# Optimization experiments

Measured on AMD Instinct MI355X. Metric: run time of the kernel, lower is better.

Reference implementation:

```python
import jax, jax.numpy as jnp
import numpy as np

B, T, N, IN_DIM, H = 8, 16, 1024, 2, 128
HEADS, HD = 8, 16            # HEADS*HD == H (DGL GATConv head-concat)
SNP, SEQ_OUT, DEG = 4, 12, 8
NT = SNP * N                 # nodes per HSTG graph
CKPNT = [4, 7, 10, 13, 16]   # _generate_checkpoints(4, 16)
LRELU = 0.2


def _build_edges():
    # HSTG: per-snapshot spatial edges (random deg-8 adjacency + self-loops)
    # plus identity temporal edges t -> t+1 (uni-direction, non-dense, sync).
    rng = np.random.default_rng(0)
    src, dst = [], []
    ar = np.arange(N)
    for t in range(SNP):
        off = t * N
        src.append(rng.integers(0, N, size=N * DEG) + off)
        dst.append(np.repeat(ar, DEG) + off)
        src.append(ar + off)   # self-loops (keep every dst non-empty)
        dst.append(ar + off)
    for t in range(SNP - 1):
        src.append(ar + t * N)
        dst.append(ar + (t + 1) * N)
    return (jnp.asarray(np.concatenate(src), dtype=jnp.int32),
            jnp.asarray(np.concatenate(dst), dtype=jnp.int32))


def setup_inputs() -> dict:
    key = jax.random.key(0)
    ks = jax.random.split(key, 16)
    edge_src, edge_dst = _build_edges()
    rn = lambda k, s, sc: jax.random.normal(k, s, dtype=jnp.float32) * sc
    return {
        'inputs': rn(ks[0], (B, T, N, IN_DIM), 1.0),
        'W_in': rn(ks[1], (IN_DIM, H), 0.5),
        'b_in': jnp.zeros((H,), jnp.float32),
        'spatial_emb': rn(ks[2], (N, H), 0.05),
        'temporal_emb': rn(ks[3], (N, T), 0.05),
        'gat_w0': rn(ks[4], (H, HEADS * HD), 0.1),
        'gat_al0': rn(ks[5], (HEADS, HD), 0.1),
        'gat_ar0': rn(ks[6], (HEADS, HD), 0.1),
        'gat_b0': jnp.zeros((HEADS * HD,), jnp.float32),
        'gat_w1': rn(ks[7], (H, HEADS * HD), 0.1),
        'gat_al1': rn(ks[8], (HEADS, HD), 0.1),
        'gat_ar1': rn(ks[9], (HEADS, HD), 0.1),
        'gat_b1': jnp.zeros((HEADS * HD,), jnp.float32),
        'agg_q': rn(ks[10], (N, H), 0.1),
        'w_out1': rn(ks[11], (1, SEQ_OUT), 0.5),
        'b_out1': jnp.zeros((SEQ_OUT,), jnp.float32),
        'w_out2': rn(ks[12], (H, 1), 0.1),
        'b_out2': jnp.zeros((1,), jnp.float32),
        'edge_src': edge_src,
        'edge_dst': edge_dst,
    }


def _gat_layer(x, W, a_l, a_r, b, src, dst, activate):
    # x: [NT, H] node features of one graph
    feat = (x @ W).reshape(NT, HEADS, HD)
    el = jnp.sum(feat * a_l, axis=-1)                 # [NT, HEADS]
    er = jnp.sum(feat * a_r, axis=-1)
    e = jax.nn.leaky_relu(el[src] + er[dst], LRELU)    # [E, HEADS]
    m = jax.ops.segment_max(e, dst, num_segments=NT)
    w = jnp.exp(e - m[dst])
    s = jax.ops.segment_sum(w, dst, num_segments=NT)
    alpha = w / s[dst]
    out = jax.ops.segment_sum(feat[src] * alpha[..., None], dst, num_segments=NT)
    out = out.reshape(NT, HEADS * HD) + b
    return jax.nn.elu(out) if activate else out


def reference(inputs, W_in, b_in, spatial_emb, temporal_emb,
              gat_w0, gat_al0, gat_ar0, gat_b0,
              gat_w1, gat_al1, gat_ar1, gat_b1,
              agg_q, w_out1, b_out1, w_out2, b_out2,
              edge_src, edge_dst):
    # input projection + spatial/temporal embeddings
    x = inputs @ W_in + b_in                           # [B,T,N,H]
    x = x + spatial_emb                                # broadcast [N,H]
    x = x + temporal_emb.T[None, :, :, None]           # add temb[n,t] at [b,t,n,h]

    def gat(xb):  # xb: [NT,H], one sample of the batched block-diagonal graph
        h = _gat_layer(xb, gat_w0, gat_al0, gat_ar0, gat_b0, edge_src, edge_dst, True)
        return _gat_layer(h, gat_w1, gat_al1, gat_ar1, gat_b1, edge_src, edge_dst, False)
    gat_b = jax.vmap(gat)

    last = None
    left = 0
    for idx, right in enumerate(CKPNT):
        fs = x[:, left:right]                          # [B, snp or snp-1, N, H]
        if idx != 0:
            fs = jnp.concatenate([last, fs], axis=1)   # [B, SNP, N, H]
        residual = fs
        h = gat_b(fs.reshape(B, NT, H)).reshape(B, SNP, N, H)
        h = h + residual
        # Aggregator: per-node attention over the SNP snapshots -> [B,1,N,H]
        scores = jnp.einsum('btnh,nh->btn', h, agg_q)
        alpha = jax.nn.softmax(scores, axis=1)
        last = jnp.einsum('btn,btnh->bnh', alpha, h)[:, None]
        # LayerNorm over normalized_shape [1,N,H], no affine
        mu = jnp.mean(last, axis=(1, 2, 3), keepdims=True)
        var = jnp.var(last, axis=(1, 2, 3), keepdims=True)
        last = (last - mu) * jax.lax.rsqrt(var + 1e-5)
        left = right

    # decoder (meta_decode = False)
    t = jnp.transpose(last, (0, 3, 2, 1))              # [B,H,N,1]
    o = jax.nn.relu(t @ w_out1 + b_out1)               # [B,H,N,SEQ_OUT]
    o = jnp.transpose(o, (0, 3, 2, 1))                 # [B,SEQ_OUT,N,H]
    return o @ w_out2 + b_out2                         # [B,SEQ_OUT,N,1]
```

## Files before the change

kernel.cpp:

```cpp
#include <hip/hip_runtime.h>
#include <hip/hip_bf16.h>
#include <math.h>

constexpr int kB = 8;
constexpr int kT = 16;
constexpr int kN = 1024;
constexpr int kH = 128;
constexpr int kSNP = 4;
constexpr int kNT = kSNP * kN;
constexpr int kRows = kB * kNT;
constexpr int kSeqOut = 12;
constexpr float kLRelu = 0.2f;
constexpr int kEdgePerSnap = kN * 8 + kN;
constexpr int kSelfOff = kN * 8;
constexpr int kTempBase = kSNP * kEdgePerSnap;
constexpr int kStatsPerIter = kB * 16 * 16;

typedef __bf16 bf16x8 __attribute__((ext_vector_type(8)));
typedef float f32x4 __attribute__((ext_vector_type(4)));

__global__ void prep_w(const float* __restrict__ gw0, const float* __restrict__ gw1,
                       unsigned short* __restrict__ wbuf) {
  int tid = blockIdx.x * 256 + threadIdx.x;
  int layer = tid >> 14;
  int e = tid & 16383;
  int k = e >> 7, col = e & 127;
  const float* W = layer ? gw1 : gw0;
  float w = W[k * kH + col];
  unsigned int bits = __float_as_uint(w);
  unsigned short hi = (unsigned short)(bits >> 16);
  float hif = __uint_as_float(bits & 0xffff0000u);
  unsigned short lo = (unsigned short)(__float_as_uint(w - hif) >> 16);
  int s = k >> 5, q = (k >> 3) & 3, j = k & 7;
  int off = ((s * 4 + q) * kH + col) * 8 + j;
  wbuf[layer * 32768 + off] = hi;
  wbuf[layer * 32768 + 16384 + off] = lo;
}

__global__ void build_fs(const float* __restrict__ inputs, const float* __restrict__ W_in,
                         const float* __restrict__ b_in, const float* __restrict__ spatial,
                         const float* __restrict__ temporal, const float* __restrict__ last,
                         const float* __restrict__ stats, float* __restrict__ A,
                         int left, int first) {
  int blk = blockIdx.x;
  int b = blk & 7;
  int inner = blk >> 3;
  int idx4 = (b << 17) | (inner << 8) | threadIdx.x;
  int h4 = idx4 & 31;
  int n  = (idx4 >> 5) & 1023;
  int t  = (idx4 >> 15) & 3;
  float4 out;
  if (!first && t == 0) {
    float s1 = 0.f, s2 = 0.f;
    #pragma unroll
    for (int s = 0; s < 16; ++s) {
      s1 += stats[b * 256 + s * 16];
      s2 += stats[b * 256 + s * 16 + 1];
    }
    const float inv = 1.0f / (float)(kN * kH);
    float mu = s1 * inv;
    float var = s2 * inv - mu * mu;
    float sc = rsqrtf(var + 1e-5f);
    float4 v = *(const float4*)(last + ((size_t)(b * kN + n)) * kH + h4 * 4);
    out.x = (v.x - mu) * sc; out.y = (v.y - mu) * sc;
    out.z = (v.z - mu) * sc; out.w = (v.w - mu) * sc;
  } else {
    int tg = left + t - (first ? 0 : 1);
    float2 iv = *(const float2*)(inputs + ((size_t)((b * kT + tg) * kN + n)) * 2);
    float tv = temporal[n * kT + tg];
    float4 w0 = *(const float4*)(W_in + h4 * 4);
    float4 w1 = *(const float4*)(W_in + kH + h4 * 4);
    float4 bb = *(const float4*)(b_in + h4 * 4);
    float4 sp = *(const float4*)(spatial + n * kH + h4 * 4);
    out.x = iv.x * w0.x + iv.y * w1.x + bb.x + sp.x + tv;
    out.y = iv.x * w0.y + iv.y * w1.y + bb.y + sp.y + tv;
    out.z = iv.x * w0.z + iv.y * w1.z + bb.z + sp.z + tv;
    out.w = iv.x * w0.w + iv.y * w1.w + bb.w + sp.w + tv;
  }
  *(float4*)(A + (size_t)idx4 * 4) = out;
}

__launch_bounds__(256)
__global__ void gemm_mfma(const float* __restrict__ In, const unsigned short* __restrict__ Wh,
                          const unsigned short* __restrict__ Wl,
                          const float* __restrict__ gal, const float* __restrict__ gar,
                          float* __restrict__ Out, float* __restrict__ elp,
                          float* __restrict__ erp) {
  __shared__ unsigned short AhL[64 * 128];
  __shared__ unsigned short AlL[64 * 128];
  int tid = threadIdx.x;
  int lane = tid & 63, wid = tid >> 6;
  int blk = blockIdx.x;
  int rowblk = ((blk & 7) << 6) | (blk >> 3);
  int blockRow0 = rowblk * 64;
  int colL = lane & 15;
  int q = lane >> 4;

  bf16x8 bh[2][4], bl[2][4];
  #pragma unroll
  for (int c = 0; c < 2; ++c) {
    int col = wid * 32 + c * 16 + colL;
    #pragma unroll
    for (int s = 0; s < 4; ++s) {
      int off = ((s * 4 + q) * kH + col) * 8;
      bh[c][s] = *(const bf16x8*)(Wh + off);
      bl[c][s] = *(const bf16x8*)(Wl + off);
    }
  }

  const float* Ablk = In + (size_t)blockRow0 * kH;
  #pragma unroll
  for (int itn = 0; itn < 8; ++itn) {
    int fid = itn * 256 + tid;
    int row = fid >> 5, kq = fid & 31;
    float4 v = *(const float4*)(Ablk + (size_t)row * kH + kq * 4);
    ushort4 hi, lo;
    unsigned int bx = __float_as_uint(v.x);
    hi.x = bx >> 16; lo.x = __float_as_uint(v.x - __uint_as_float(bx & 0xffff0000u)) >> 16;
    unsigned int by = __float_as_uint(v.y);
    hi.y = by >> 16; lo.y = __float_as_uint(v.y - __uint_as_float(by & 0xffff0000u)) >> 16;
    unsigned int bz = __float_as_uint(v.z);
    hi.z = bz >> 16; lo.z = __float_as_uint(v.z - __uint_as_float(bz & 0xffff0000u)) >> 16;
    unsigned int bw = __float_as_uint(v.w);
    hi.w = bw >> 16; lo.w = __float_as_uint(v.w - __uint_as_float(bw & 0xffff0000u)) >> 16;
    int boff = (row * 256 + kq * 8) ^ ((row & 7) << 4);
    *(ushort4*)((char*)AhL + boff) = hi;
    *(ushort4*)((char*)AlL + boff) = lo;
  }
  __syncthreads();

  f32x4 acc[4][2];
  #pragma unroll
  for (int rb = 0; rb < 4; ++rb)
    #pragma unroll
    for (int c = 0; c < 2; ++c) acc[rb][c] = (f32x4){0.f, 0.f, 0.f, 0.f};

  #pragma unroll
  for (int s = 0; s < 4; ++s) {
    bf16x8 ah[4], alr[4];
    #pragma unroll
    for (int rb = 0; rb < 4; ++rb) {
      int row = rb * 16 + colL;
      int boff = (row * 256 + s * 64 + q * 16) ^ ((row & 7) << 4);
      ah[rb]  = *(const bf16x8*)((const char*)AhL + boff);
      alr[rb] = *(const bf16x8*)((const char*)AlL + boff);
    }
    #pragma unroll
    for (int c = 0; c < 2; ++c) {
      #pragma unroll
      for (int rb = 0; rb < 4; ++rb)
        acc[rb][c] = __builtin_amdgcn_mfma_f32_16x16x32_bf16(ah[rb], bh[c][s], acc[rb][c], 0, 0, 0);
      #pragma unroll
      for (int rb = 0; rb < 4; ++rb)
        acc[rb][c] = __builtin_amdgcn_mfma_f32_16x16x32_bf16(alr[rb], bh[c][s], acc[rb][c], 0, 0, 0);
      #pragma unroll
      for (int rb = 0; rb < 4; ++rb)
        acc[rb][c] = __builtin_amdgcn_mfma_f32_16x16x32_bf16(ah[rb], bl[c][s], acc[rb][c], 0, 0, 0);
    }
  }

  int rquad = q * 4;
  #pragma unroll
  for (int c = 0; c < 2; ++c) {
    int h = wid * 2 + c;
    float alv = gal[h * 16 + colL];
    float arv = gar[h * 16 + colL];
    int col = wid * 32 + c * 16 + colL;
    #pragma unroll
    for (int rb = 0; rb < 4; ++rb) {
      f32x4 a = acc[rb][c];
      int row0g = blockRow0 + rb * 16 + rquad;
      #pragma unroll
      for (int r = 0; r < 4; ++r)
        Out[(size_t)(row0g + r) * kH + col] = a[r];
      float e0 = a[0] * alv, e1 = a[1] * alv, e2 = a[2] * alv, e3 = a[3] * alv;
      float f0 = a[0] * arv, f1 = a[1] * arv, f2 = a[2] * arv, f3 = a[3] * arv;
      #pragma unroll
      for (int m = 1; m < 16; m <<= 1) {
        e0 += __shfl_xor(e0, m, 64); e1 += __shfl_xor(e1, m, 64);
        e2 += __shfl_xor(e2, m, 64); e3 += __shfl_xor(e3, m, 64);
        f0 += __shfl_xor(f0, m, 64); f1 += __shfl_xor(f1, m, 64);
        f2 += __shfl_xor(f2, m, 64); f3 += __shfl_xor(f3, m, 64);
      }
      if (colL == 0) {
        elp[(size_t)(row0g + 0) * 8 + h] = e0;
        elp[(size_t)(row0g + 1) * 8 + h] = e1;
        elp[(size_t)(row0g + 2) * 8 + h] = e2;
        elp[(size_t)(row0g + 3) * 8 + h] = e3;
        erp[(size_t)(row0g + 0) * 8 + h] = f0;
        erp[(size_t)(row0g + 1) * 8 + h] = f1;
        erp[(size_t)(row0g + 2) * 8 + h] = f2;
        erp[(size_t)(row0g + 3) * 8 + h] = f3;
      }
    }
  }
}

__launch_bounds__(256)
__global__ void agg0_kernel(const float* __restrict__ feat, const float* __restrict__ el,
                            const float* __restrict__ er, const int* __restrict__ esrc,
                            const float* __restrict__ bias, float* __restrict__ outp) {
  int blk = blockIdx.x;
  int b = blk & 7;
  int grp = blk >> 3;
  int tid = threadIdx.x;
  int wave = tid >> 6, lane = tid & 63;
  int v = grp * 4 + wave;
  int t = v >> 10, n = v & 1023;
  int h = lane >> 3;
  int bv = (b << 12) + v;

  int srcs[10];
  int base8 = t * kEdgePerSnap + n * 8;
  #pragma unroll
  for (int k = 0; k < 8; ++k) srcs[k] = esrc[base8 + k];
  srcs[8] = esrc[t * kEdgePerSnap + kSelfOff + n];
  float erv = er[bv * 8 + h];
  int ebase = b << 15;

  float e[10];
  float m = -1e30f;
  #pragma unroll
  for (int i = 0; i < 9; ++i) {
    float x = el[ebase + srcs[i] * 8 + h] + erv;
    x = x > 0.f ? x : kLRelu * x;
    e[i] = x;
    m = fmaxf(m, x);
  }
  if (t > 0) {
    int s9 = esrc[kTempBase + (t - 1) * kN + n];
    srcs[9] = s9;
    float x = el[ebase + s9 * 8 + h] + erv;
    x = x > 0.f ? x : kLRelu * x;
    e[9] = x;
    m = fmaxf(m, x);
  } else {
    srcs[9] = v;
    e[9] = -1e30f;
  }
  float s = 0.f;
  #pragma unroll
  for (int i = 0; i < 10; ++i) { e[i] = expf(e[i] - m); s += e[i]; }
  float inv = 1.0f / s;

  float ax = 0.f, ay = 0.f;
  size_t fbase = (size_t)(b << 12) * kH;
  #pragma unroll
  for (int i = 0; i < 10; ++i) {
    float w = e[i] * inv;
    float2 fv = *(const float2*)(feat + fbase + (size_t)srcs[i] * kH + lane * 2);
    ax += w * fv.x;
    ay += w * fv.y;
  }
  float2 bb = *(const float2*)(bias + lane * 2);
  float x0 = ax + bb.x, x1 = ay + bb.y;
  float2 o;
  o.x = x0 > 0.f ? x0 : expm1f(x0);
  o.y = x1 > 0.f ? x1 : expm1f(x1);
  *(float2*)(outp + (size_t)bv * kH + lane * 2) = o;
}

__launch_bounds__(256)
__global__ void agg1_attn(const float* __restrict__ feat, const float* __restrict__ el,
                          const float* __restrict__ er, const int* __restrict__ esrc,
                          const float* __restrict__ bias, const float* __restrict__ resid,
                          const float* __restrict__ q, float* __restrict__ last,
                          float* __restrict__ stats) {
  __shared__ float ssc[4];
  __shared__ float hbuf[4][128];
  __shared__ float sred[4];
  int blk = blockIdx.x;
  int b = blk & 7;
  int n = blk >> 3;
  int tid = threadIdx.x;
  int t = tid >> 6, lane = tid & 63;
  int v = (t << 10) + n;
  int h = lane >> 3;
  int bv = (b << 12) + v;

  int srcs[10];
  int base8 = t * kEdgePerSnap + n * 8;
  #pragma unroll
  for (int k = 0; k < 8; ++k) srcs[k] = esrc[base8 + k];
  srcs[8] = esrc[t * kEdgePerSnap + kSelfOff + n];
  float erv = er[bv * 8 + h];
  int ebase = b << 15;

  float e[10];
  float m = -1e30f;
  #pragma unroll
  for (int i = 0; i < 9; ++i) {
    float x = el[ebase + srcs[i] * 8 + h] + erv;
    x = x > 0.f ? x : kLRelu * x;
    e[i] = x;
    m = fmaxf(m, x);
  }
  if (t > 0) {
    int s9 = esrc[kTempBase + (t - 1) * kN + n];
    srcs[9] = s9;
    float x = el[ebase + s9 * 8 + h] + erv;
    x = x > 0.f ? x : kLRelu * x;
    e[9] = x;
    m = fmaxf(m, x);
  } else {
    srcs[9] = v;
    e[9] = -1e30f;
  }
  float s = 0.f;
  #pragma unroll
  for (int i = 0; i < 10; ++i) { e[i] = expf(e[i] - m); s += e[i]; }
  float inv = 1.0f / s;

  float ax = 0.f, ay = 0.f;
  size_t fbase = (size_t)(b << 12) * kH;
  #pragma unroll
  for (int i = 0; i < 10; ++i) {
    float w = e[i] * inv;
    float2 fv = *(const float2*)(feat + fbase + (size_t)srcs[i] * kH + lane * 2);
    ax += w * fv.x;
    ay += w * fv.y;
  }
  float2 bb = *(const float2*)(bias + lane * 2);
  float2 rv = *(const float2*)(resid + (size_t)bv * kH + lane * 2);
  float hx = ax + bb.x + rv.x;
  float hy = ay + bb.y + rv.y;

  float2 qv = *(const float2*)(q + (size_t)n * kH + lane * 2);
  float p = hx * qv.x + hy * qv.y;
  #pragma unroll
  for (int s_ = 1; s_ < 64; s_ <<= 1) p += __shfl_xor(p, s_, 64);
  if (lane == 0) ssc[t] = p;
  __syncthreads();
  float s0 = ssc[0], s1 = ssc[1], s2 = ssc[2], s3 = ssc[3];
  float mm = fmaxf(fmaxf(s0, s1), fmaxf(s2, s3));
  float a0 = expf(s0 - mm), a1 = expf(s1 - mm), a2 = expf(s2 - mm), a3 = expf(s3 - mm);
  float denom = 1.0f / (a0 + a1 + a2 + a3);
  float at = (t == 0 ? a0 : t == 1 ? a1 : t == 2 ? a2 : a3) * denom;
  hbuf[t][lane * 2]     = hx * at;
  hbuf[t][lane * 2 + 1] = hy * at;
  __syncthreads();

  float p1 = 0.f, p2 = 0.f;
  if (tid < 128) {
    int d = tid;
    float sum = hbuf[0][d] + hbuf[1][d] + hbuf[2][d] + hbuf[3][d];
    last[((size_t)(b * kN + n)) * kH + d] = sum;
    p1 = sum;
    p2 = sum * sum;
  }
  #pragma unroll
  for (int s_ = 1; s_ < 64; s_ <<= 1) {
    p1 += __shfl_xor(p1, s_, 64);
    p2 += __shfl_xor(p2, s_, 64);
  }
  if (tid < 128 && lane == 0) { sred[t * 2] = p1; sred[t * 2 + 1] = p2; }
  __syncthreads();
  if (tid == 0) {
    int slot = n & 15;
    atomicAdd(&stats[b * 256 + slot * 16],     sred[0] + sred[2]);
    atomicAdd(&stats[b * 256 + slot * 16 + 1], sred[1] + sred[3]);
  }
}

__global__ void out_kernel(const float* __restrict__ last, const float* __restrict__ stats,
                           const float* __restrict__ w1, const float* __restrict__ b1,
                           const float* __restrict__ w2, const float* __restrict__ b2,
                           float* __restrict__ out) {
  int tid = threadIdx.x;
  int wave = tid >> 6, lane = tid & 63;
  int gw = blockIdx.x * 4 + wave;
  int b = gw >> 10, n = gw & 1023;
  float s1 = 0.f, s2 = 0.f;
  #pragma unroll
  for (int s = 0; s < 16; ++s) {
    s1 += stats[b * 256 + s * 16];
    s2 += stats[b * 256 + s * 16 + 1];
  }
  const float inv = 1.0f / (float)(kN * kH);
  float mu = s1 * inv;
  float var = s2 * inv - mu * mu;
  float scv = rsqrtf(var + 1e-5f);
  int d0 = lane * 2;
  float2 lv = *(const float2*)(last + ((size_t)(b * kN + n)) * kH + d0);
  float x0 = (lv.x - mu) * scv, x1 = (lv.y - mu) * scv;
  float w20 = w2[d0], w21 = w2[d0 + 1];
  float bias2 = b2[0];
  #pragma unroll
  for (int s = 0; s < kSeqOut; ++s) {
    float w1s = w1[s], b1s = b1[s];
    float v = fmaxf(x0 * w1s + b1s, 0.f) * w20 + fmaxf(x1 * w1s + b1s, 0.f) * w21;
    #pragma unroll
    for (int k = 1; k < 64; k <<= 1) v += __shfl_xor(v, k, 64);
    if (lane == 0) out[(size_t)(b * kSeqOut + s) * kN + n] = v + bias2;
  }
}

extern "C" void kernel_launch(void* const* d_in, const int* in_sizes, int n_in,
                              void* d_out, int out_size, void* d_ws, size_t ws_size,
                              hipStream_t stream) {
  const float* inputs   = (const float*)d_in[0];
  const float* W_in     = (const float*)d_in[1];
  const float* b_in     = (const float*)d_in[2];
  const float* spatial  = (const float*)d_in[3];
  const float* temporal = (const float*)d_in[4];
  const float* gw0      = (const float*)d_in[5];
  const float* gal0     = (const float*)d_in[6];
  const float* gar0     = (const float*)d_in[7];
  const float* gb0      = (const float*)d_in[8];
  const float* gw1      = (const float*)d_in[9];
  const float* gal1     = (const float*)d_in[10];
  const float* gar1     = (const float*)d_in[11];
  const float* gb1      = (const float*)d_in[12];
  const float* aggq     = (const float*)d_in[13];
  const float* w_out1   = (const float*)d_in[14];
  const float* b_out1   = (const float*)d_in[15];
  const float* w_out2   = (const float*)d_in[16];
  const float* b_out2   = (const float*)d_in[17];
  const int*   esrc     = (const int*)d_in[18];

  float* ws = (float*)d_ws;
  float* A     = ws;
  float* Bf    = ws + 4194304;
  float* C     = ws + 8388608;
  float* el    = ws + 12582912;
  float* er    = ws + 12845056;
  float* last  = ws + 13107200;
  float* stats = ws + 14155776;
  unsigned short* wsplit = (unsigned short*)(ws + 14166016);

  hipMemsetAsync(stats, 0, 5 * kStatsPerIter * sizeof(float), stream);
  prep_w<<<128, 256, 0, stream>>>(gw0, gw1, wsplit);
  const unsigned short* w0h = wsplit;
  const unsigned short* w0l = wsplit + 16384;
  const unsigned short* w1h = wsplit + 32768;
  const unsigned short* w1l = wsplit + 49152;

  const int lefts[5] = {0, 4, 7, 10, 13};
  for (int it = 0; it < 5; ++it) {
    const float* st_prev = (it == 0) ? stats : (stats + (it - 1) * kStatsPerIter);
    build_fs<<<4096, 256, 0, stream>>>(inputs, W_in, b_in, spatial, temporal,
                                       last, st_prev, A, lefts[it], it == 0 ? 1 : 0);
    gemm_mfma<<<kRows / 64, 256, 0, stream>>>(A, w0h, w0l, gal0, gar0, Bf, el, er);
    agg0_kernel<<<8192, 256, 0, stream>>>(Bf, el, er, esrc, gb0, C);
    gemm_mfma<<<kRows / 64, 256, 0, stream>>>(C, w1h, w1l, gal1, gar1, Bf, el, er);
    agg1_attn<<<8192, 256, 0, stream>>>(Bf, el, er, esrc, gb1, A, aggq, last,
                                        stats + it * kStatsPerIter);
  }
  out_kernel<<<2048, 256, 0, stream>>>(last, stats + 4 * kStatsPerIter, w_out1, b_out1,
                                       w_out2, b_out2, (float*)d_out);
}
```

Measured before the change: 510.0 us.

## Fuse input construction into first GEMM and recompute residual in attention aggregation

Removes the separate build_fs kernel. The first-layer GEMM now builds its input tile on the fly, either from the input embedding or from the layer-normalized previous state, before splitting it to bf16 hi/lo. The agg1 kernel recomputes the residual the same way instead of reading a materialized A buffer. This removes a full write and two full reads of the intermediate tensor plus one launch per checkpoint iteration, at the cost of some redundant embedding and stats arithmetic.

```diff
diff --git a/kernel.cpp b/kernel.cpp
--- a/kernel.cpp
+++ b/kernel.cpp
@@ -37,62 +37,26 @@
   wbuf[layer * 32768 + 16384 + off] = lo;
 }
 
-__global__ void build_fs(const float* __restrict__ inputs, const float* __restrict__ W_in,
-                         const float* __restrict__ b_in, const float* __restrict__ spatial,
-                         const float* __restrict__ temporal, const float* __restrict__ last,
-                         const float* __restrict__ stats, float* __restrict__ A,
-                         int left, int first) {
-  int blk = blockIdx.x;
-  int b = blk & 7;
-  int inner = blk >> 3;
-  int idx4 = (b << 17) | (inner << 8) | threadIdx.x;
-  int h4 = idx4 & 31;
-  int n  = (idx4 >> 5) & 1023;
-  int t  = (idx4 >> 15) & 3;
-  float4 out;
-  if (!first && t == 0) {
-    float s1 = 0.f, s2 = 0.f;
-    #pragma unroll
-    for (int s = 0; s < 16; ++s) {
-      s1 += stats[b * 256 + s * 16];
-      s2 += stats[b * 256 + s * 16 + 1];
-    }
-    const float inv = 1.0f / (float)(kN * kH);
-    float mu = s1 * inv;
-    float var = s2 * inv - mu * mu;
-    float sc = rsqrtf(var + 1e-5f);
-    float4 v = *(const float4*)(last + ((size_t)(b * kN + n)) * kH + h4 * 4);
-    out.x = (v.x - mu) * sc; out.y = (v.y - mu) * sc;
-    out.z = (v.z - mu) * sc; out.w = (v.w - mu) * sc;
-  } else {
-    int tg = left + t - (first ? 0 : 1);
-    float2 iv = *(const float2*)(inputs + ((size_t)((b * kT + tg) * kN + n)) * 2);
-    float tv = temporal[n * kT + tg];
-    float4 w0 = *(const float4*)(W_in + h4 * 4);
-    float4 w1 = *(const float4*)(W_in + kH + h4 * 4);
-    float4 bb = *(const float4*)(b_in + h4 * 4);
-    float4 sp = *(const float4*)(spatial + n * kH + h4 * 4);
-    out.x = iv.x * w0.x + iv.y * w1.x + bb.x + sp.x + tv;
-    out.y = iv.x * w0.y + iv.y * w1.y + bb.y + sp.y + tv;
-    out.z = iv.x * w0.z + iv.y * w1.z + bb.z + sp.z + tv;
-    out.w = iv.x * w0.w + iv.y * w1.w + bb.w + sp.w + tv;
-  }
-  *(float4*)(A + (size_t)idx4 * 4) = out;
-}
-
+template <int BUILD>
 __launch_bounds__(256)
-__global__ void gemm_mfma(const float* __restrict__ In, const unsigned short* __restrict__ Wh,
+__global__ void gemm_mfma(const float* __restrict__ In,
+                          const unsigned short* __restrict__ Wh,
                           const unsigned short* __restrict__ Wl,
                           const float* __restrict__ gal, const float* __restrict__ gar,
                           float* __restrict__ Out, float* __restrict__ elp,
-                          float* __restrict__ erp) {
+                          float* __restrict__ erp,
+                          const float* __restrict__ inputs, const float* __restrict__ W_in,
+                          const float* __restrict__ b_in, const float* __restrict__ spatial,
+                          const float* __restrict__ temporal, const float* __restrict__ last,
+                          const float* __restrict__ stats, int left, int first) {
   __shared__ unsigned short AhL[64 * 128];
   __shared__ unsigned short AlL[64 * 128];
   int tid = threadIdx.x;
   int lane = tid & 63, wid = tid >> 6;
   int blk = blockIdx.x;
-  int rowblk = ((blk & 7) << 6) | (blk >> 3);
-  int blockRow0 = rowblk * 64;
+  int b = blk & 7;
+  int inner = blk >> 3;
+  int blockRow0 = (b << 12) + inner * 64;
   int colL = lane & 15;
   int q = lane >> 4;
 
@@ -108,12 +72,50 @@
     }
   }
 
+  int tblk = inner >> 4;
+  int nbase = (inner & 15) << 6;
+  float mu = 0.f, scn = 0.f;
+  bool lnpath = BUILD && !first && tblk == 0;
+  if (lnpath) {
+    float s1 = 0.f, s2 = 0.f;
+    #pragma unroll
+    for (int s = 0; s < 16; ++s) {
+      s1 += stats[b * 256 + s * 16];
+      s2 += stats[b * 256 + s * 16 + 1];
+    }
+    const float inv = 1.0f / (float)(kN * kH);
+    mu = s1 * inv;
+    float var = s2 * inv - mu * mu;
+    scn = rsqrtf(var + 1e-5f);
+  }
   const float* Ablk = In + (size_t)blockRow0 * kH;
   #pragma unroll
   for (int itn = 0; itn < 8; ++itn) {
     int fid = itn * 256 + tid;
     int row = fid >> 5, kq = fid & 31;
-    float4 v = *(const float4*)(Ablk + (size_t)row * kH + kq * 4);
+    float4 v;
+    if (BUILD) {
+      int n = nbase + row;
+      if (lnpath) {
+        float4 lv = *(const float4*)(last + ((size_t)(b * kN + n)) * kH + kq * 4);
+        v.x = (lv.x - mu) * scn; v.y = (lv.y - mu) * scn;
+        v.z = (lv.z - mu) * scn; v.w = (lv.w - mu) * scn;
+      } else {
+        int tg = left + tblk - (first ? 0 : 1);
+        float2 iv = *(const float2*)(inputs + ((size_t)((b * kT + tg) * kN + n)) * 2);
+        float tv = temporal[n * kT + tg];
+        float4 w0 = *(const float4*)(W_in + kq * 4);
+        float4 w1 = *(const float4*)(W_in + kH + kq * 4);
+        float4 bb = *(const float4*)(b_in + kq * 4);
+        float4 sp = *(const float4*)(spatial + (size_t)n * kH + kq * 4);
+        v.x = iv.x * w0.x + iv.y * w1.x + bb.x + sp.x + tv;
+        v.y = iv.x * w0.y + iv.y * w1.y + bb.y + sp.y + tv;
+        v.z = iv.x * w0.z + iv.y * w1.z + bb.z + sp.z + tv;
+        v.w = iv.x * w0.w + iv.y * w1.w + bb.w + sp.w + tv;
+      }
+    } else {
+      v = *(const float4*)(Ablk + (size_t)row * kH + kq * 4);
+    }
     ushort4 hi, lo;
     unsigned int bx = __float_as_uint(v.x);
     hi.x = bx >> 16; lo.x = __float_as_uint(v.x - __uint_as_float(bx & 0xffff0000u)) >> 16;
@@ -263,12 +265,15 @@
 __launch_bounds__(256)
 __global__ void agg1_attn(const float* __restrict__ feat, const float* __restrict__ el,
                           const float* __restrict__ er, const int* __restrict__ esrc,
-                          const float* __restrict__ bias, const float* __restrict__ resid,
-                          const float* __restrict__ q, float* __restrict__ last,
-                          float* __restrict__ stats) {
+                          const float* __restrict__ bias, const float* __restrict__ q,
+                          float* __restrict__ last, float* __restrict__ stats,
+                          const float* __restrict__ inputs, const float* __restrict__ W_in,
+                          const float* __restrict__ b_in, const float* __restrict__ spatial,
+                          const float* __restrict__ temporal,
+                          const float* __restrict__ st_prev, int left, int first) {
   __shared__ float ssc[4];
   __shared__ float hbuf[4][128];
-  __shared__ float sred[4];
+  __shared__ float sred[8];
   int blk = blockIdx.x;
   int b = blk & 7;
   int n = blk >> 3;
@@ -321,11 +326,34 @@
     ay += w * fv.y;
   }
   float2 bb = *(const float2*)(bias + lane * 2);
-  float2 rv = *(const float2*)(resid + (size_t)bv * kH + lane * 2);
-  float hx = ax + bb.x + rv.x;
-  float hy = ay + bb.y + rv.y;
-
-  float2 qv = *(const float2*)(q + (size_t)n * kH + lane * 2);
+
+  int d0 = lane * 2;
+  float rx, ry;
+  if (!first && t == 0) {
+    float s1 = 0.f, s2 = 0.f;
+    #pragma unroll
+    for (int ss = 0; ss < 16; ++ss) {
+      s1 += st_prev[b * 256 + ss * 16];
+      s2 += st_prev[b * 256 + ss * 16 + 1];
+    }
+    const float invq = 1.0f / (float)(kN * kH);
+    float muq = s1 * invq;
+    float varq = s2 * invq - muq * muq;
+    float scq = rsqrtf(varq + 1e-5f);
+    float2 lv = *(const float2*)(last + ((size_t)(b * kN + n)) * kH + d0);
+    rx = (lv.x - muq) * scq;
+    ry = (lv.y - muq) * scq;
+  } else {
+    int tg = left + t - (first ? 0 : 1);
+    float2 iv = *(const float2*)(inputs + ((size_t)((b * kT + tg) * kN + n)) * 2);
+    float tv = temporal[n * kT + tg];
+    rx = iv.x * W_in[d0]     + iv.y * W_in[kH + d0]     + b_in[d0]     + spatial[(size_t)n * kH + d0]     + tv;
+    ry = iv.x * W_in[d0 + 1] + iv.y * W_in[kH + d0 + 1] + b_in[d0 + 1] + spatial[(size_t)n * kH + d0 + 1] + tv;
+  }
+  float hx = ax + bb.x + rx;
+  float hy = ay + bb.y + ry;
+
+  float2 qv = *(const float2*)(q + (size_t)n * kH + d0);
   float p = hx * qv.x + hy * qv.y;
   #pragma unroll
   for (int s_ = 1; s_ < 64; s_ <<= 1) p += __shfl_xor(p, s_, 64);
@@ -336,8 +364,8 @@
   float a0 = expf(s0 - mm), a1 = expf(s1 - mm), a2 = expf(s2 - mm), a3 = expf(s3 - mm);
   float denom = 1.0f / (a0 + a1 + a2 + a3);
   float at = (t == 0 ? a0 : t == 1 ? a1 : t == 2 ? a2 : a3) * denom;
-  hbuf[t][lane * 2]     = hx * at;
-  hbuf[t][lane * 2 + 1] = hy * at;
+  hbuf[t][d0]     = hx * at;
+  hbuf[t][d0 + 1] = hy * at;
   __syncthreads();
 
   float p1 = 0.f, p2 = 0.f;
@@ -419,14 +447,13 @@
   const int*   esrc     = (const int*)d_in[18];
 
   float* ws = (float*)d_ws;
-  float* A     = ws;
-  float* Bf    = ws + 4194304;
-  float* C     = ws + 8388608;
-  float* el    = ws + 12582912;
-  float* er    = ws + 12845056;
-  float* last  = ws + 13107200;
-  float* stats = ws + 14155776;
-  unsigned short* wsplit = (unsigned short*)(ws + 14166016);
+  float* Bf    = ws;
+  float* C     = ws + 4194304;
+  float* el    = ws + 8388608;
+  float* er    = ws + 8650752;
+  float* last  = ws + 8912896;
+  float* stats = ws + 9961472;
+  unsigned short* wsplit = (unsigned short*)(ws + 9971712);
 
   hipMemsetAsync(stats, 0, 5 * kStatsPerIter * sizeof(float), stream);
   prep_w<<<128, 256, 0, stream>>>(gw0, gw1, wsplit);
@@ -438,13 +465,18 @@
   const int lefts[5] = {0, 4, 7, 10, 13};
   for (int it = 0; it < 5; ++it) {
     const float* st_prev = (it == 0) ? stats : (stats + (it - 1) * kStatsPerIter);
-    build_fs<<<4096, 256, 0, stream>>>(inputs, W_in, b_in, spatial, temporal,
-                                       last, st_prev, A, lefts[it], it == 0 ? 1 : 0);
-    gemm_mfma<<<kRows / 64, 256, 0, stream>>>(A, w0h, w0l, gal0, gar0, Bf, el, er);
+    int first = (it == 0) ? 1 : 0;
+    gemm_mfma<1><<<kRows / 64, 256, 0, stream>>>(
+        nullptr, w0h, w0l, gal0, gar0, Bf, el, er,
+        inputs, W_in, b_in, spatial, temporal, last, st_prev, lefts[it], first);
     agg0_kernel<<<8192, 256, 0, stream>>>(Bf, el, er, esrc, gb0, C);
-    gemm_mfma<<<kRows / 64, 256, 0, stream>>>(C, w1h, w1l, gal1, gar1, Bf, el, er);
-    agg1_attn<<<8192, 256, 0, stream>>>(Bf, el, er, esrc, gb1, A, aggq, last,
-                                        stats + it * kStatsPerIter);
+    gemm_mfma<0><<<kRows / 64, 256, 0, stream>>>(
+        C, w1h, w1l, gal1, gar1, Bf, el, er,
+        inputs, W_in, b_in, spatial, temporal, last, st_prev, 0, 1);
+    agg1_attn<<<8192, 256, 0, stream>>>(Bf, el, er, esrc, gb1, aggq, last,
+                                        stats + it * kStatsPerIter,
+                                        inputs, W_in, b_in, spatial, temporal,
+                                        st_prev, lefts[it], first);
   }
   out_kernel<<<2048, 256, 0, stream>>>(last, stats + 4 * kStatsPerIter, w_out1, b_out1,
                                        w_out2, b_out2, (float*)d_out);
```

Result: slower. 530.4 us (+4.0%).
